# Kernel optimization log

Measured on AMD Instinct MI355X. Metric: run time of the kernel, lower is better.

The kernel has to match this reference:

```python
import jax, jax.numpy as jnp
import numpy as np

A, B, S, ADIM = 8, 8192, 128, 16   # n_agents, batch, state_dim, act_dim
H, HEADS = 512, 4                   # hidc, att_heads
D = H // HEADS                      # att_dim
EPS = 1e-5


def _ln(x):
    # LayerNorm over last dim, no affine (elementwise_affine=False), eps=1e-5
    m = jnp.mean(x, axis=-1, keepdims=True)
    v = jnp.var(x, axis=-1, keepdims=True)
    return (x - m) * jax.lax.rsqrt(v + EPS)


def setup_inputs() -> dict:
    key = jax.random.key(0)
    ks = jax.random.split(key, 16)
    sc = 0.02
    return {
        "states": jax.random.normal(ks[0], (A, B, S), jnp.float32),
        "actions": jax.random.normal(ks[1], (A, B, ADIM), jnp.float32),
        # per-agent state encoders (Encoder built with hidc in the source)
        "Ws_s": jax.random.normal(ks[2], (A, S, H), jnp.float32) * sc,
        "bs_s": jnp.zeros((A, H), jnp.float32),
        # per-agent state-action encoders
        "Ws_sa": jax.random.normal(ks[3], (A, S + ADIM, H), jnp.float32) * sc,
        "bs_sa": jnp.zeros((A, H), jnp.float32),
        # shared per-head key/value/selector projections
        "Wk": jax.random.normal(ks[4], (HEADS, H, D), jnp.float32) * sc,
        "Wv": jax.random.normal(ks[5], (HEADS, H, D), jnp.float32) * sc,
        "Wsel": jax.random.normal(ks[6], (HEADS, H, D), jnp.float32) * sc,
        "bsel": jnp.zeros((HEADS, D), jnp.float32),
        # per-agent critics: Linear(2H -> H), LeakyReLU, Linear(H -> ADIM)
        "Wc1": jax.random.normal(ks[7], (A, 2 * H, H), jnp.float32) * sc,
        "bc1": jnp.zeros((A, H), jnp.float32),
        "Wc2": jax.random.normal(ks[8], (A, H, ADIM), jnp.float32) * sc,
        "bc2": jnp.zeros((A, ADIM), jnp.float32),
    }


def reference(states, actions, Ws_s, bs_s, Ws_sa, bs_sa,
              Wk, Wv, Wsel, bsel, Wc1, bc1, Wc2, bc2):
    lrelu = jax.nn.leaky_relu  # slope 0.01 matches torch default

    # per-agent state encodings: [A,B,H]
    s_enc = lrelu(jnp.einsum('abs,ash->abh', _ln(states), Ws_s) + bs_s[:, None, :])

    # per-agent state-action encodings: [A,B,H]
    sa = jnp.concatenate([states, actions], axis=-1)
    sa_enc = lrelu(jnp.einsum('abs,ash->abh', _ln(sa), Ws_sa) + bs_sa[:, None, :])

    # per-head keys / values / selectors: [HEADS, A, B, D]
    keys = jnp.einsum('abh,khd->kabd', sa_enc, Wk)
    vals = jnp.einsum('abh,khd->kabd', sa_enc, Wv)
    sel = lrelu(jnp.einsum('abh,khd->kabd', sa_enc, Wsel) + bsel[:, None, None, :])

    # attention logits of agent i over agents j != i: [HEADS, A, A, B]
    logits = jnp.einsum('kibd,kjbd->kijb', sel, keys) / np.sqrt(D).astype(np.float32)
    self_mask = jnp.eye(A, dtype=bool)[None, :, :, None]
    w = jax.nn.softmax(jnp.where(self_mask, -jnp.inf, logits), axis=2)

    # attended values: [HEADS, A, B, D] -> concat heads -> [A, B, H]
    qvals = jnp.einsum('kijb,kjbd->kibd', w, vals)
    values = qvals.transpose(1, 2, 0, 3).reshape(A, B, H)

    # per-agent critics on concat(state_enc, attended values)
    cin = jnp.concatenate([s_enc, values], axis=-1)           # [A,B,2H]
    h1 = lrelu(jnp.einsum('abf,afh->abh', _ln(cin), Wc1) + bc1[:, None, :])
    all_qs = jnp.einsum('abh,aho->abo', h1, Wc2) + bc2[:, None, :]  # [A,B,ADIM]

    # Q of taken (argmax) action per agent: [A,B,1]
    idx = jnp.argmax(actions, axis=-1)
    q = jnp.take_along_axis(all_qs, idx[..., None], axis=-1)
    return q
```

## Files before the change

kernel.cpp:

```cpp
#include <hip/hip_runtime.h>
#include <hip/hip_bf16.h>
#include <math.h>


#define AN 8
#define BNB 8192
#define SN 128
#define ADN 16
#define HN 512
#define NHEADS 4
#define DN 128

typedef __hip_bfloat16 bf16;
typedef unsigned short u16;
typedef __attribute__((ext_vector_type(8))) short bf16x8;
typedef __attribute__((ext_vector_type(4))) float f32x4;

__device__ __forceinline__ float lrelu(float x){ return x > 0.f ? x : 0.01f*x; }
__device__ __forceinline__ float bflo(unsigned u){ return __uint_as_float(u << 16); }
__device__ __forceinline__ float bfhi(unsigned u){ return __uint_as_float(u & 0xffff0000u); }
__device__ __forceinline__ float bf2f(u16 u){ return __uint_as_float((unsigned)u << 16); }
__device__ __forceinline__ u16 f2bf(float v){
  union { bf16 h; u16 s; } cv; cv.h = __float2bfloat16(v); return cv.s;
}
__device__ __forceinline__ ushort4 f4bf(float4 v){
  ushort4 u; u.x=f2bf(v.x); u.y=f2bf(v.y); u.z=f2bf(v.z); u.w=f2bf(v.w); return u;
}

__device__ __forceinline__ void gload16(const u16* g, u16* l){
  __builtin_amdgcn_global_load_lds(
      (const __attribute__((address_space(1))) unsigned int*)(g),
      (__attribute__((address_space(3))) unsigned int*)(l), 16, 0, 0);
}

__global__ __launch_bounds__(256) void prep_kernel(
    const float* __restrict__ states, const float* __restrict__ actions,
    u16* __restrict__ sa_bf, float2* __restrict__ st_s, float2* __restrict__ st_sa,
    int* __restrict__ aip)
{
  const int lane = threadIdx.x & 63;
  const int r = blockIdx.x*4 + (threadIdx.x >> 6);
  float2 sv = ((const float2*)(states + (size_t)r*SN))[lane];
  float s1 = sv.x + sv.y, q1 = sv.x*sv.x + sv.y*sv.y;
  float2 av = make_float2(0.f, 0.f);
  if (lane < 8) av = ((const float2*)(actions + (size_t)r*ADN))[lane];
  float s2 = s1 + av.x + av.y, q2 = q1 + av.x*av.x + av.y*av.y;
  #pragma unroll
  for (int off=32; off; off>>=1){
    s1 += __shfl_xor(s1,off); q1 += __shfl_xor(q1,off);
    s2 += __shfl_xor(s2,off); q2 += __shfl_xor(q2,off);
  }
  float bv; int bi;
  if (lane < 8){
    if (av.x >= av.y){ bv = av.x; bi = 2*lane; } else { bv = av.y; bi = 2*lane+1; }
  } else { bv = -INFINITY; bi = 999; }
  #pragma unroll
  for (int off=1; off<8; off<<=1){
    float ov = __shfl_xor(bv, off); int oi = __shfl_xor(bi, off);
    if (ov > bv || (ov == bv && oi < bi)){ bv = ov; bi = oi; }
  }
  u16* row = sa_bf + (size_t)r*192;
  ushort2 p; p.x = f2bf(sv.x); p.y = f2bf(sv.y);
  *(ushort2*)(row + 2*lane) = p;
  if (lane < 8){
    ushort2 pa; pa.x = f2bf(av.x); pa.y = f2bf(av.y);
    *(ushort2*)(row + 128 + 2*lane) = pa;
  } else if (lane < 32){
    ushort2 z; z.x = 0; z.y = 0;
    *(ushort2*)(row + 128 + 2*lane) = z;
  }
  if (lane==0){
    float m1 = s1*(1.f/128.f), v1 = fmaxf(q1*(1.f/128.f)-m1*m1, 0.f);
    st_s[r] = make_float2(m1, rsqrtf(v1+1e-5f));
    float m2 = s2*(1.f/144.f), v2 = fmaxf(q2*(1.f/144.f)-m2*m2, 0.f);
    st_sa[r] = make_float2(m2, rsqrtf(v2+1e-5f));
    aip[r] = bi;
  }
}

__global__ __launch_bounds__(256) void transw_all_kernel(
    const float* __restrict__ Ws_s, const float* __restrict__ Ws_sa, const float* __restrict__ Wc1,
    const float* __restrict__ Wk, const float* __restrict__ Wv, const float* __restrict__ Wsel,
    u16* __restrict__ Wt_s, u16* __restrict__ Wt_sa, u16* __restrict__ Wt_c1, u16* __restrict__ Wt_p)
{
  __shared__ float t[32][33];
  int id = blockIdx.x;
  const float* in; u16* outp; int K, Kp; size_t zs; int gx;
  const int N = (id < 5376) ? 512 : 128;
  if (id < 512){            in=Ws_s;  outp=Wt_s;            K=128;  Kp=128;  zs=(size_t)512*128;  gx=4;  }
  else if (id < 1280){ id-=512;  in=Ws_sa; outp=Wt_sa;      K=144;  Kp=192;  zs=(size_t)512*192;  gx=6;  }
  else if (id < 5376){ id-=1280; in=Wc1;   outp=Wt_c1;      K=1024; Kp=1024; zs=(size_t)512*1024; gx=32; }
  else if (id < 5632){ id-=5376; in=Wk;    outp=Wt_p;            K=512; Kp=512; zs=(size_t)3*128*512; gx=16; }
  else if (id < 5888){ id-=5632; in=Wv;    outp=Wt_p+128*512;    K=512; Kp=512; zs=(size_t)3*128*512; gx=16; }
  else {               id-=5888; in=Wsel;  outp=Wt_p+2*128*512;  K=512; Kp=512; zs=(size_t)3*128*512; gx=16; }
  const int bx = id % gx; id /= gx;
  const int gy = N >> 5;
  const int by = id % gy;
  const int z  = id / gy;
  const int tx = threadIdx.x, ty = threadIdx.y;
  const int k0 = bx*32, n0 = by*32;
  const float* ip = in + (size_t)z*K*N;
  #pragma unroll
  for (int i=0;i<4;i++){
    int k = k0 + ty*4 + i;
    t[ty*4+i][tx] = (k < K) ? ip[(size_t)k*N + n0 + tx] : 0.f;
  }
  __syncthreads();
  u16* op = outp + (size_t)z*zs;
  #pragma unroll
  for (int i=0;i<4;i++){
    int n = n0 + ty*4 + i;
    op[(size_t)n*Kp + k0 + tx] = f2bf(t[tx][ty*4+i]);
  }
}

__global__ __launch_bounds__(256) void colsum_bf_kernel(
    const u16* __restrict__ Wt_s, const u16* __restrict__ Wt_sa, const u16* __restrict__ Wt_c1,
    float* __restrict__ cs_s, float* __restrict__ cs_sa, float* __restrict__ cs_c1)
{
  const int lane = threadIdx.x & 63;
  const int row = blockIdx.x*4 + (threadIdx.x >> 6);
  const int which = row >> 12; const int idx = row & 4095;
  const u16* W; int K; float* outp;
  if (which==0){ W = Wt_s;  K = 128;  outp = cs_s;  }
  else if (which==1){ W = Wt_sa; K = 192;  outp = cs_sa; }
  else { W = Wt_c1; K = 1024; outp = cs_c1; }
  const u16* p = W + (size_t)idx*K;
  float s = 0.f;
  for (int c = lane*8; c < K; c += 512){
    uint4 v = *(const uint4*)(p + c);
    const unsigned w4[4] = {v.x, v.y, v.z, v.w};
    #pragma unroll
    for (int t=0;t<4;t++) s += bflo(w4[t]) + bfhi(w4[t]);
  }
  #pragma unroll
  for (int off=32; off; off>>=1) s += __shfl_xor(s,off);
  if (lane==0) outp[idx] = s;
}

template<int MODE>
__global__ __launch_bounds__(256) void mfma_enc_kernel(
    const u16* __restrict__ Aa, const u16* __restrict__ Ab,
    const u16* __restrict__ Wt, const float* __restrict__ bias,
    const float2* __restrict__ stats, const float* __restrict__ csum,
    u16* __restrict__ outp,
    const float* __restrict__ Wc2, const float* __restrict__ bc2,
    const int* __restrict__ aip, float* __restrict__ qout)
{
  constexpr int K   = (MODE==0) ? 128 : (MODE==1 ? 192 : 1024);
  constexpr int LDA = (MODE==2) ? 512 : 192;
  constexpr int KP  = K;
  constexpr int SMEMN = (MODE==2) ? 20736 : 17408;
  __shared__ __align__(16) u16 smem[SMEMN];
  u16* As = smem;
  u16* Bs = smem + 8192;
  const int tid = threadIdx.x;
  const int w = tid>>6, lane = tid&63;
  const int wr = w>>1, wc = w&1;
  const int srow = lane>>3, skq = (lane&7)^srow;

  const int nwg = gridDim.x * gridDim.y;
  int id = blockIdx.y * gridDim.x + blockIdx.x;
  int swz = (id & 7) * (nwg >> 3) + (id >> 3);
  const int bx = swz % gridDim.x, by = swz / gridDim.x;

  const int m0 = by*128, n0c = bx*128;
  const int a = by >> 6;
  const u16* Wbase = Wt + (size_t)a*HN*KP;
  const int slotbase = (lane>>4) ^ (lane&7);
  f32x4 acc[4][4] = {};

  float* wc2l = nullptr; int* ail = nullptr;
  if constexpr (MODE==2){
    wc2l = (float*)(smem + 16384);
    ail  = (int*)(smem + 16384 + 4096);
    for (int e = tid; e < 2048; e += 256){
      const int aidx = e >> 7, col = e & 127;
      wc2l[e] = Wc2[((size_t)a*HN + n0c + col)*ADN + aidx];
    }
    if (tid < 128) ail[tid] = aip[m0 + tid];
  }

  for (int k0 = 0; k0 < K; k0 += 64){
    __syncthreads();
    const u16* asrc; int acol;
    if (MODE==2){ asrc = (k0 < 512) ? Aa : Ab; acol = k0 & 511; }
    else        { asrc = Aa; acol = k0; }
    #pragma unroll
    for (int t=0;t<4;t++){
      const int rr = w*32 + t*8;
      gload16(asrc  + (size_t)(m0  + rr + srow)*LDA + acol + skq*8, As + rr*64);
      gload16(Wbase + (size_t)(n0c + rr + srow)*KP  + k0   + skq*8, Bs + rr*64);
    }
    __syncthreads();
    #pragma unroll
    for (int ks=0; ks<2; ++ks){
      bf16x8 af[4], bv[4];
      const int so = ((slotbase ^ (ks<<2)))*8;
      #pragma unroll
      for (int mi=0;mi<4;mi++) af[mi] = *(const bf16x8*)&As[(wr*64+mi*16+(lane&15))*64 + so];
      #pragma unroll
      for (int ni=0;ni<4;ni++) bv[ni] = *(const bf16x8*)&Bs[(wc*64+ni*16+(lane&15))*64 + so];
      #pragma unroll
      for (int mi=0;mi<4;mi++)
        #pragma unroll
        for (int ni=0;ni<4;ni++)
          acc[mi][ni] = __builtin_amdgcn_mfma_f32_16x16x32_bf16(af[mi], bv[ni], acc[mi][ni], 0, 0, 0);
    }
  }

  __syncthreads();
  float csv[4], biv[4];
  #pragma unroll
  for (int ni=0;ni<4;ni++){
    const int col = n0c + wc*64 + ni*16 + (lane&15);
    csv[ni] = csum[a*HN + col];
    biv[ni] = bias[a*HN + col];
  }

  if constexpr (MODE==2){
    #pragma unroll
    for (int mi=0;mi<4;mi++){
      const int rbase = wr*64 + mi*16 + ((lane>>4)<<2);
      #pragma unroll
      for (int v=0; v<4; ++v){
        const int rl = rbase + v;
        const float2 st = stats[m0 + rl];
        const int aidx = ail[rl];
        float p = 0.f;
        #pragma unroll
        for (int ni=0;ni<4;ni++){
          const int coll = wc*64 + ni*16 + (lane&15);
          const float o = lrelu(st.y*(acc[mi][ni][v] - st.x*csv[ni]) + biv[ni]);
          p = fmaf(o, wc2l[aidx*128 + coll], p);
        }
        p += __shfl_xor(p,1); p += __shfl_xor(p,2);
        p += __shfl_xor(p,4); p += __shfl_xor(p,8);
        if ((lane&15)==0){
          if (n0c==0 && wc==0) p += bc2[a*ADN + aidx];
          atomicAdd(qout + m0 + rl, p);
        }
      }
    }
  } else {
    #pragma unroll
    for (int mi=0;mi<4;mi++){
      const int rl = wr*64 + mi*16 + ((lane>>4)<<2);
      #pragma unroll
      for (int v=0; v<4; ++v){
        const float2 st = stats[m0 + rl + v];
        #pragma unroll
        for (int ni=0;ni<4;ni++){
          const float o = lrelu(st.y*(acc[mi][ni][v] - st.x*csv[ni]) + biv[ni]);
          smem[(rl+v)*136 + wc*64 + ni*16 + (lane&15)] = f2bf(o);
        }
      }
    }
    __syncthreads();
    #pragma unroll
    for (int it=0; it<8; ++it){
      const int rl = it*16 + (tid>>4);
      const int ck = (tid&15)*8;
      const uint4 vv = *(const uint4*)&smem[rl*136 + ck];
      *(uint4*)(outp + (size_t)(m0+rl)*HN + n0c + ck) = vv;
    }
  }
}

__global__ __launch_bounds__(256) void mfma_proj_kernel(
    const u16* __restrict__ sa_enc, const u16* __restrict__ Wt_p,
    const float* __restrict__ bsel, u16* __restrict__ kvs, int head)
{
  __shared__ __align__(16) u16 smem[17408];
  u16* As = smem;
  u16* Bs = smem + 8192;
  const int tid = threadIdx.x;
  const int w = tid>>6, lane = tid&63;
  const int wr = w>>1, wc = w&1;
  const int srow = lane>>3, skq = (lane&7)^srow;

  const int nwg = gridDim.x * gridDim.y;
  int id = blockIdx.y * gridDim.x + blockIdx.x;
  int swz = (id & 7) * (nwg >> 3) + (id >> 3);
  const int t = swz % gridDim.x;
  const int m0 = (swz / gridDim.x) * 128;

  const u16* Wbase = Wt_p + (size_t)(head*3 + t)*DN*HN;
  const int slotbase = (lane>>4) ^ (lane&7);
  f32x4 acc[4][4] = {};

  for (int k0 = 0; k0 < HN; k0 += 64){
    __syncthreads();
    #pragma unroll
    for (int tt=0;tt<4;tt++){
      const int rr = w*32 + tt*8;
      gload16(sa_enc + (size_t)(m0 + rr + srow)*HN + k0 + skq*8, As + rr*64);
      gload16(Wbase  + (size_t)(rr + srow)*HN      + k0 + skq*8, Bs + rr*64);
    }
    __syncthreads();
    #pragma unroll
    for (int ks=0; ks<2; ++ks){
      bf16x8 af[4], bv[4];
      const int so = ((slotbase ^ (ks<<2)))*8;
      #pragma unroll
      for (int mi=0;mi<4;mi++) af[mi] = *(const bf16x8*)&As[(wr*64+mi*16+(lane&15))*64 + so];
      #pragma unroll
      for (int ni=0;ni<4;ni++) bv[ni] = *(const bf16x8*)&Bs[(wc*64+ni*16+(lane&15))*64 + so];
      #pragma unroll
      for (int mi=0;mi<4;mi++)
        #pragma unroll
        for (int ni=0;ni<4;ni++)
          acc[mi][ni] = __builtin_amdgcn_mfma_f32_16x16x32_bf16(af[mi], bv[ni], acc[mi][ni], 0, 0, 0);
    }
  }

  __syncthreads();
  const bool issel = (t == 2);
  float biv[4];
  #pragma unroll
  for (int ni=0;ni<4;ni++){
    const int col = wc*64 + ni*16 + (lane&15);
    biv[ni] = issel ? bsel[head*DN + col] : 0.f;
  }
  #pragma unroll
  for (int mi=0;mi<4;mi++){
    const int rl = wr*64 + mi*16 + ((lane>>4)<<2);
    #pragma unroll
    for (int v=0; v<4; ++v){
      #pragma unroll
      for (int ni=0;ni<4;ni++){
        float o = acc[mi][ni][v] + biv[ni];
        if (issel) o = lrelu(o);
        smem[(rl+v)*136 + wc*64 + ni*16 + (lane&15)] = f2bf(o);
      }
    }
  }
  __syncthreads();
  #pragma unroll
  for (int it=0; it<8; ++it){
    const int rl = it*16 + (tid>>4);
    const int ck = (tid&15)*8;
    const int r = m0 + rl;
    const int ar = r >> 13, b = r & (BNB-1);
    const uint4 vv = *(const uint4*)&smem[rl*136 + ck];
    *(uint4*)(kvs + (((size_t)t*BNB + b)*AN + ar)*DN + ck) = vv;
  }
}

__global__ __launch_bounds__(256) void attn_kernel(
    const u16* __restrict__ kvs, u16* __restrict__ values, int kh)
{
  __shared__ float lds[4][3232];
  const int lane = threadIdx.x & 63;
  const int wv   = threadIdx.x >> 6;
  float* selL = &lds[wv][0];
  float* keyL = &lds[wv][1056];
  float* valL = &lds[wv][2112];
  float* wL   = &lds[wv][3168];
  const int b = blockIdx.x*4 + wv;

  #pragma unroll
  for (int m=0;m<3;m++){
    const int t = (m==0) ? 2 : ((m==1) ? 0 : 1);
    float* dst = (m==0) ? selL : ((m==1) ? keyL : valL);
    const uint2* p = (const uint2*)(kvs + ((size_t)t*BNB + b)*(AN*DN));
    #pragma unroll
    for (int it=0; it<4; it++){
      uint2 u = p[it*64 + lane];
      int e = (it*64 + lane)*4;
      int j = e >> 7, d = e & 127;
      float4 f;
      f.x = bflo(u.x); f.y = bfhi(u.x); f.z = bflo(u.y); f.w = bfhi(u.y);
      *(float4*)&dst[j*132 + d] = f;
    }
  }
  __syncthreads();

  const int i = lane >> 3, j = lane & 7;
  float acc = 0.f;
  #pragma unroll 8
  for (int dq=0; dq<32; dq++){
    const float4 s4 = *(const float4*)&selL[i*132 + dq*4];
    const float4 k4 = *(const float4*)&keyL[j*132 + dq*4];
    acc += s4.x*k4.x + s4.y*k4.y + s4.z*k4.z + s4.w*k4.w;
  }
  float logit = acc * 0.08838834764831845f;
  if (i == j) logit = -INFINITY;
  float mx = logit;
  mx = fmaxf(mx, __shfl_xor(mx,1,8));
  mx = fmaxf(mx, __shfl_xor(mx,2,8));
  mx = fmaxf(mx, __shfl_xor(mx,4,8));
  const float e = __expf(logit - mx);
  float s = e;
  s += __shfl_xor(s,1,8);
  s += __shfl_xor(s,2,8);
  s += __shfl_xor(s,4,8);
  wL[i*8 + j] = e / s;
  __syncthreads();

  const int dq = lane & 7;
  float4 o[4];
  #pragma unroll
  for (int tt=0;tt<4;tt++) o[tt] = make_float4(0.f,0.f,0.f,0.f);
  #pragma unroll
  for (int jj=0;jj<8;jj++){
    const float wj = wL[i*8 + jj];
    #pragma unroll
    for (int tt=0;tt<4;tt++){
      const float4 v4 = *(const float4*)&valL[jj*132 + tt*32 + dq*4];
      o[tt].x += wj*v4.x; o[tt].y += wj*v4.y; o[tt].z += wj*v4.z; o[tt].w += wj*v4.w;
    }
  }
  u16* dst = values + ((size_t)i*BNB + b)*HN + kh*DN;
  #pragma unroll
  for (int tt=0;tt<4;tt++)
    *(ushort4*)(dst + tt*32 + dq*4) = f4bf(o[tt]);
}

__global__ __launch_bounds__(256) void stats_cin_kernel(
    const u16* __restrict__ s_enc, const u16* __restrict__ values, float2* __restrict__ st)
{
  const int lane = threadIdx.x & 63;
  const int r = blockIdx.x*4 + (threadIdx.x >> 6);
  const uint4* p1 = (const uint4*)(s_enc + (size_t)r*HN);
  const uint4* p2 = (const uint4*)(values + (size_t)r*HN);
  uint4 va = p1[lane];
  uint4 vb = p2[lane];
  float s=0.f, q=0.f;
  const unsigned wa[4] = {va.x, va.y, va.z, va.w};
  const unsigned wb[4] = {vb.x, vb.y, vb.z, vb.w};
  #pragma unroll
  for (int t=0;t<4;t++){
    float f0 = bflo(wa[t]), f1 = bfhi(wa[t]);
    float g0 = bflo(wb[t]), g1 = bfhi(wb[t]);
    s += f0+f1+g0+g1; q += f0*f0+f1*f1+g0*g0+g1*g1;
  }
  #pragma unroll
  for (int off=32; off; off>>=1){ s += __shfl_xor(s,off); q += __shfl_xor(q,off); }
  if (lane==0){
    float m = s*(1.f/1024.f); float v = fmaxf(q*(1.f/1024.f) - m*m, 0.f);
    st[r] = make_float2(m, rsqrtf(v + 1e-5f));
  }
}

extern "C" void kernel_launch(void* const* d_in, const int* in_sizes, int n_in,
                              void* d_out, int out_size, void* d_ws, size_t ws_size,
                              hipStream_t stream)
{
  (void)in_sizes; (void)n_in; (void)ws_size;
  const float* states  = (const float*)d_in[0];
  const float* actions = (const float*)d_in[1];
  const float* Ws_s    = (const float*)d_in[2];
  const float* bs_s    = (const float*)d_in[3];
  const float* Ws_sa   = (const float*)d_in[4];
  const float* bs_sa   = (const float*)d_in[5];
  const float* Wk      = (const float*)d_in[6];
  const float* Wv      = (const float*)d_in[7];
  const float* Wsel    = (const float*)d_in[8];
  const float* bsel    = (const float*)d_in[9];
  const float* Wc1     = (const float*)d_in[10];
  const float* bc1     = (const float*)d_in[11];
  const float* Wc2     = (const float*)d_in[12];
  const float* bc2     = (const float*)d_in[13];
  float* outp = (float*)d_out;

  char* ws = (char*)d_ws;
  size_t off = 0;
  auto alloc = [&](size_t n){ void* p = ws + off; off += (n + 255) & ~(size_t)255; return p; };
  u16*    slot1  = (u16*)   alloc((size_t)AN*BNB*HN*2);
  u16*    s_enc  = slot1;
  u16*    kvs    = slot1;
  u16*    sa_enc = (u16*)   alloc((size_t)AN*BNB*HN*2);
  u16*    values = (u16*)   alloc((size_t)AN*BNB*HN*2);
  u16*    sa_bf  = (u16*)   alloc((size_t)AN*BNB*192*2);
  u16*    Wt_s   = (u16*)   alloc((size_t)AN*HN*128*2);
  u16*    Wt_sa  = (u16*)   alloc((size_t)AN*HN*192*2);
  u16*    Wt_c1  = (u16*)   alloc((size_t)AN*HN*1024*2);
  u16*    Wt_p   = (u16*)   alloc((size_t)NHEADS*3*DN*HN*2);
  float2* st_s   = (float2*)alloc((size_t)AN*BNB*8);
  float2* st_sa  = (float2*)alloc((size_t)AN*BNB*8);
  float2* st_cin = (float2*)alloc((size_t)AN*BNB*8);
  float*  cs_s   = (float*) alloc((size_t)AN*HN*4);
  float*  cs_sa  = (float*) alloc((size_t)AN*HN*4);
  float*  cs_c1  = (float*) alloc((size_t)AN*HN*4);
  int*    aip    = (int*)   alloc((size_t)AN*BNB*4);

  hipMemsetAsync(d_out, 0, (size_t)out_size*4, stream);
  prep_kernel<<<dim3(AN*BNB/4), 256, 0, stream>>>(states, actions, sa_bf, st_s, st_sa, aip);
  transw_all_kernel<<<dim3(6144), dim3(32,8), 0, stream>>>(
      Ws_s, Ws_sa, Wc1, Wk, Wv, Wsel, Wt_s, Wt_sa, Wt_c1, Wt_p);
  colsum_bf_kernel<<<dim3(3*AN*HN/4), 256, 0, stream>>>(Wt_s, Wt_sa, Wt_c1, cs_s, cs_sa, cs_c1);

  mfma_enc_kernel<1><<<dim3(4,512), 256, 0, stream>>>(sa_bf, nullptr, Wt_sa, bs_sa, st_sa, cs_sa,
                                                      sa_enc, nullptr, nullptr, nullptr, nullptr);
  for (int kh = 0; kh < NHEADS; ++kh){
    mfma_proj_kernel<<<dim3(3,512), 256, 0, stream>>>(sa_enc, Wt_p, bsel, kvs, kh);
    attn_kernel<<<dim3(BNB/4), 256, 0, stream>>>(kvs, values, kh);
  }
  mfma_enc_kernel<0><<<dim3(4,512), 256, 0, stream>>>(sa_bf, nullptr, Wt_s, bs_s, st_s, cs_s,
                                                      s_enc, nullptr, nullptr, nullptr, nullptr);
  stats_cin_kernel<<<dim3(AN*BNB/4), 256, 0, stream>>>(s_enc, values, st_cin);
  mfma_enc_kernel<2><<<dim3(4,512), 256, 0, stream>>>(s_enc, values, Wt_c1, bc1, st_cin, cs_c1,
                                                      nullptr, Wc2, bc2, aip, outp);
}
```

Baseline: 471.7 us.

## Split critic GEMM into dedicated kernel and keep attention tiles in bf16 LDS

```diff
diff --git a/kernel.cpp b/kernel.cpp
--- a/kernel.cpp
+++ b/kernel.cpp
@@ -23,8 +23,8 @@
 __device__ __forceinline__ u16 f2bf(float v){
   union { bf16 h; u16 s; } cv; cv.h = __float2bfloat16(v); return cv.s;
 }
-__device__ __forceinline__ ushort4 f4bf(float4 v){
-  ushort4 u; u.x=f2bf(v.x); u.y=f2bf(v.y); u.z=f2bf(v.z); u.w=f2bf(v.w); return u;
+__device__ __forceinline__ unsigned pk2(float a, float b){
+  return (unsigned)f2bf(a) | ((unsigned)f2bf(b) << 16);
 }
 
 __device__ __forceinline__ void gload16(const u16* g, u16* l){
@@ -140,137 +140,14 @@
 
 template<int MODE>
 __global__ __launch_bounds__(256) void mfma_enc_kernel(
-    const u16* __restrict__ Aa, const u16* __restrict__ Ab,
+    const u16* __restrict__ Aa,
     const u16* __restrict__ Wt, const float* __restrict__ bias,
     const float2* __restrict__ stats, const float* __restrict__ csum,
-    u16* __restrict__ outp,
-    const float* __restrict__ Wc2, const float* __restrict__ bc2,
-    const int* __restrict__ aip, float* __restrict__ qout)
-{
-  constexpr int K   = (MODE==0) ? 128 : (MODE==1 ? 192 : 1024);
-  constexpr int LDA = (MODE==2) ? 512 : 192;
+    u16* __restrict__ outp)
+{
+  constexpr int K   = (MODE==0) ? 128 : 192;
+  constexpr int LDA = 192;
   constexpr int KP  = K;
-  constexpr int SMEMN = (MODE==2) ? 20736 : 17408;
-  __shared__ __align__(16) u16 smem[SMEMN];
-  u16* As = smem;
-  u16* Bs = smem + 8192;
-  const int tid = threadIdx.x;
-  const int w = tid>>6, lane = tid&63;
-  const int wr = w>>1, wc = w&1;
-  const int srow = lane>>3, skq = (lane&7)^srow;
-
-  const int nwg = gridDim.x * gridDim.y;
-  int id = blockIdx.y * gridDim.x + blockIdx.x;
-  int swz = (id & 7) * (nwg >> 3) + (id >> 3);
-  const int bx = swz % gridDim.x, by = swz / gridDim.x;
-
-  const int m0 = by*128, n0c = bx*128;
-  const int a = by >> 6;
-  const u16* Wbase = Wt + (size_t)a*HN*KP;
-  const int slotbase = (lane>>4) ^ (lane&7);
-  f32x4 acc[4][4] = {};
-
-  float* wc2l = nullptr; int* ail = nullptr;
-  if constexpr (MODE==2){
-    wc2l = (float*)(smem + 16384);
-    ail  = (int*)(smem + 16384 + 4096);
-    for (int e = tid; e < 2048; e += 256){
-      const int aidx = e >> 7, col = e & 127;
-      wc2l[e] = Wc2[((size_t)a*HN + n0c + col)*ADN + aidx];
-    }
-    if (tid < 128) ail[tid] = aip[m0 + tid];
-  }
-
-  for (int k0 = 0; k0 < K; k0 += 64){
-    __syncthreads();
-    const u16* asrc; int acol;
-    if (MODE==2){ asrc = (k0 < 512) ? Aa : Ab; acol = k0 & 511; }
-    else        { asrc = Aa; acol = k0; }
-    #pragma unroll
-    for (int t=0;t<4;t++){
-      const int rr = w*32 + t*8;
-      gload16(asrc  + (size_t)(m0  + rr + srow)*LDA + acol + skq*8, As + rr*64);
-      gload16(Wbase + (size_t)(n0c + rr + srow)*KP  + k0   + skq*8, Bs + rr*64);
-    }
-    __syncthreads();
-    #pragma unroll
-    for (int ks=0; ks<2; ++ks){
-      bf16x8 af[4], bv[4];
-      const int so = ((slotbase ^ (ks<<2)))*8;
-      #pragma unroll
-      for (int mi=0;mi<4;mi++) af[mi] = *(const bf16x8*)&As[(wr*64+mi*16+(lane&15))*64 + so];
-      #pragma unroll
-      for (int ni=0;ni<4;ni++) bv[ni] = *(const bf16x8*)&Bs[(wc*64+ni*16+(lane&15))*64 + so];
-      #pragma unroll
-      for (int mi=0;mi<4;mi++)
-        #pragma unroll
-        for (int ni=0;ni<4;ni++)
-          acc[mi][ni] = __builtin_amdgcn_mfma_f32_16x16x32_bf16(af[mi], bv[ni], acc[mi][ni], 0, 0, 0);
-    }
-  }
-
-  __syncthreads();
-  float csv[4], biv[4];
-  #pragma unroll
-  for (int ni=0;ni<4;ni++){
-    const int col = n0c + wc*64 + ni*16 + (lane&15);
-    csv[ni] = csum[a*HN + col];
-    biv[ni] = bias[a*HN + col];
-  }
-
-  if constexpr (MODE==2){
-    #pragma unroll
-    for (int mi=0;mi<4;mi++){
-      const int rbase = wr*64 + mi*16 + ((lane>>4)<<2);
-      #pragma unroll
-      for (int v=0; v<4; ++v){
-        const int rl = rbase + v;
-        const float2 st = stats[m0 + rl];
-        const int aidx = ail[rl];
-        float p = 0.f;
-        #pragma unroll
-        for (int ni=0;ni<4;ni++){
-          const int coll = wc*64 + ni*16 + (lane&15);
-          const float o = lrelu(st.y*(acc[mi][ni][v] - st.x*csv[ni]) + biv[ni]);
-          p = fmaf(o, wc2l[aidx*128 + coll], p);
-        }
-        p += __shfl_xor(p,1); p += __shfl_xor(p,2);
-        p += __shfl_xor(p,4); p += __shfl_xor(p,8);
-        if ((lane&15)==0){
-          if (n0c==0 && wc==0) p += bc2[a*ADN + aidx];
-          atomicAdd(qout + m0 + rl, p);
-        }
-      }
-    }
-  } else {
-    #pragma unroll
-    for (int mi=0;mi<4;mi++){
-      const int rl = wr*64 + mi*16 + ((lane>>4)<<2);
-      #pragma unroll
-      for (int v=0; v<4; ++v){
-        const float2 st = stats[m0 + rl + v];
-        #pragma unroll
-        for (int ni=0;ni<4;ni++){
-          const float o = lrelu(st.y*(acc[mi][ni][v] - st.x*csv[ni]) + biv[ni]);
-          smem[(rl+v)*136 + wc*64 + ni*16 + (lane&15)] = f2bf(o);
-        }
-      }
-    }
-    __syncthreads();
-    #pragma unroll
-    for (int it=0; it<8; ++it){
-      const int rl = it*16 + (tid>>4);
-      const int ck = (tid&15)*8;
-      const uint4 vv = *(const uint4*)&smem[rl*136 + ck];
-      *(uint4*)(outp + (size_t)(m0+rl)*HN + n0c + ck) = vv;
-    }
-  }
-}
-
-__global__ __launch_bounds__(256) void mfma_proj_kernel(
-    const u16* __restrict__ sa_enc, const u16* __restrict__ Wt_p,
-    const float* __restrict__ bsel, u16* __restrict__ kvs, int head)
-{
   __shared__ __align__(16) u16 smem[17408];
   u16* As = smem;
   u16* Bs = smem + 8192;
@@ -282,6 +159,178 @@
   const int nwg = gridDim.x * gridDim.y;
   int id = blockIdx.y * gridDim.x + blockIdx.x;
   int swz = (id & 7) * (nwg >> 3) + (id >> 3);
+  const int bx = swz % gridDim.x, by = swz / gridDim.x;
+
+  const int m0 = by*128, n0c = bx*128;
+  const int a = by >> 6;
+  const u16* Wbase = Wt + (size_t)a*HN*KP;
+  const int slotbase = (lane>>4) ^ (lane&7);
+  f32x4 acc[4][4] = {};
+
+  for (int k0 = 0; k0 < K; k0 += 64){
+    __syncthreads();
+    #pragma unroll
+    for (int t=0;t<4;t++){
+      const int rr = w*32 + t*8;
+      gload16(Aa    + (size_t)(m0  + rr + srow)*LDA + k0 + skq*8, As + rr*64);
+      gload16(Wbase + (size_t)(n0c + rr + srow)*KP  + k0 + skq*8, Bs + rr*64);
+    }
+    __syncthreads();
+    #pragma unroll
+    for (int ks=0; ks<2; ++ks){
+      bf16x8 af[4], bv[4];
+      const int so = ((slotbase ^ (ks<<2)))*8;
+      #pragma unroll
+      for (int mi=0;mi<4;mi++) af[mi] = *(const bf16x8*)&As[(wr*64+mi*16+(lane&15))*64 + so];
+      #pragma unroll
+      for (int ni=0;ni<4;ni++) bv[ni] = *(const bf16x8*)&Bs[(wc*64+ni*16+(lane&15))*64 + so];
+      #pragma unroll
+      for (int mi=0;mi<4;mi++)
+        #pragma unroll
+        for (int ni=0;ni<4;ni++)
+          acc[mi][ni] = __builtin_amdgcn_mfma_f32_16x16x32_bf16(af[mi], bv[ni], acc[mi][ni], 0, 0, 0);
+    }
+  }
+
+  __syncthreads();
+  float csv[4], biv[4];
+  #pragma unroll
+  for (int ni=0;ni<4;ni++){
+    const int col = n0c + wc*64 + ni*16 + (lane&15);
+    csv[ni] = csum[a*HN + col];
+    biv[ni] = bias[a*HN + col];
+  }
+  #pragma unroll
+  for (int mi=0;mi<4;mi++){
+    const int rl = wr*64 + mi*16 + ((lane>>4)<<2);
+    #pragma unroll
+    for (int v=0; v<4; ++v){
+      const float2 st = stats[m0 + rl + v];
+      #pragma unroll
+      for (int ni=0;ni<4;ni++){
+        const float o = lrelu(st.y*(acc[mi][ni][v] - st.x*csv[ni]) + biv[ni]);
+        smem[(rl+v)*136 + wc*64 + ni*16 + (lane&15)] = f2bf(o);
+      }
+    }
+  }
+  __syncthreads();
+  #pragma unroll
+  for (int it=0; it<8; ++it){
+    const int rl = it*16 + (tid>>4);
+    const int ck = (tid&15)*8;
+    const uint4 vv = *(const uint4*)&smem[rl*136 + ck];
+    *(uint4*)(outp + (size_t)(m0+rl)*HN + n0c + ck) = vv;
+  }
+}
+
+__global__ __launch_bounds__(256, 4) void mfma_critic_kernel(
+    const u16* __restrict__ Aa, const u16* __restrict__ Ab,
+    const u16* __restrict__ Wt, const float* __restrict__ bias,
+    const float2* __restrict__ stats, const float* __restrict__ csum,
+    const float* __restrict__ Wc2, const float* __restrict__ bc2,
+    const int* __restrict__ aip, float* __restrict__ qout)
+{
+  __shared__ __align__(16) u16 smem[18688];
+  u16* As = smem;
+  u16* Bs = smem + 8192;
+  u16* wc2l = smem + 16384;
+  int* ail  = (int*)(smem + 18432);
+  const int tid = threadIdx.x;
+  const int w = tid>>6, lane = tid&63;
+  const int wr = w>>1, wc = w&1;
+  const int srow = lane>>3, skq = (lane&7)^srow;
+
+  const int nwg = gridDim.x * gridDim.y;
+  int id = blockIdx.y * gridDim.x + blockIdx.x;
+  int swz = (id & 7) * (nwg >> 3) + (id >> 3);
+  const int bx = swz % gridDim.x, by = swz / gridDim.x;
+
+  const int m0 = by*128, n0c = bx*128;
+  const int a = by >> 6;
+  const u16* Wbase = Wt + (size_t)a*HN*1024;
+  const int slotbase = (lane>>4) ^ (lane&7);
+  f32x4 acc[4][4] = {};
+
+  const float* wsrc = Wc2 + ((size_t)a*HN + n0c)*ADN;
+  #pragma unroll
+  for (int i = 0; i < 8; ++i) wc2l[i*256 + tid] = f2bf(wsrc[i*256 + tid]);
+  if (tid < 128) ail[tid] = aip[m0 + tid];
+
+  for (int k0 = 0; k0 < 1024; k0 += 64){
+    __syncthreads();
+    const u16* asrc = (k0 < 512) ? Aa : Ab;
+    const int acol = k0 & 511;
+    #pragma unroll
+    for (int t=0;t<4;t++){
+      const int rr = w*32 + t*8;
+      gload16(asrc  + (size_t)(m0  + rr + srow)*HN   + acol + skq*8, As + rr*64);
+      gload16(Wbase + (size_t)(n0c + rr + srow)*1024 + k0   + skq*8, Bs + rr*64);
+    }
+    __syncthreads();
+    #pragma unroll
+    for (int ks=0; ks<2; ++ks){
+      bf16x8 af[4], bv[4];
+      const int so = ((slotbase ^ (ks<<2)))*8;
+      #pragma unroll
+      for (int mi=0;mi<4;mi++) af[mi] = *(const bf16x8*)&As[(wr*64+mi*16+(lane&15))*64 + so];
+      #pragma unroll
+      for (int ni=0;ni<4;ni++) bv[ni] = *(const bf16x8*)&Bs[(wc*64+ni*16+(lane&15))*64 + so];
+      #pragma unroll
+      for (int mi=0;mi<4;mi++)
+        #pragma unroll
+        for (int ni=0;ni<4;ni++)
+          acc[mi][ni] = __builtin_amdgcn_mfma_f32_16x16x32_bf16(af[mi], bv[ni], acc[mi][ni], 0, 0, 0);
+    }
+  }
+
+  __syncthreads();
+  float csv[4], biv[4];
+  #pragma unroll
+  for (int ni=0;ni<4;ni++){
+    const int col = n0c + wc*64 + ni*16 + (lane&15);
+    csv[ni] = csum[a*HN + col];
+    biv[ni] = bias[a*HN + col];
+  }
+  #pragma unroll
+  for (int mi=0;mi<4;mi++){
+    const int rbase = wr*64 + mi*16 + ((lane>>4)<<2);
+    #pragma unroll
+    for (int v=0; v<4; ++v){
+      const int rl = rbase + v;
+      const float2 st = stats[m0 + rl];
+      const int aidx = ail[rl];
+      float p = 0.f;
+      #pragma unroll
+      for (int ni=0;ni<4;ni++){
+        const int coll = wc*64 + ni*16 + (lane&15);
+        const float o = lrelu(st.y*(acc[mi][ni][v] - st.x*csv[ni]) + biv[ni]);
+        p = fmaf(o, bf2f(wc2l[coll*16 + aidx]), p);
+      }
+      p += __shfl_xor(p,1); p += __shfl_xor(p,2);
+      p += __shfl_xor(p,4); p += __shfl_xor(p,8);
+      if ((lane&15)==0){
+        if (n0c==0 && wc==0) p += bc2[a*ADN + aidx];
+        atomicAdd(qout + m0 + rl, p);
+      }
+    }
+  }
+}
+
+__global__ __launch_bounds__(256) void mfma_proj_kernel(
+    const u16* __restrict__ sa_enc, const u16* __restrict__ Wt_p,
+    const float* __restrict__ bsel, u16* __restrict__ kvs, int head)
+{
+  __shared__ __align__(16) u16 smem[17408];
+  u16* As = smem;
+  u16* Bs = smem + 8192;
+  const int tid = threadIdx.x;
+  const int w = tid>>6, lane = tid&63;
+  const int wr = w>>1, wc = w&1;
+  const int srow = lane>>3, skq = (lane&7)^srow;
+
+  const int nwg = gridDim.x * gridDim.y;
+  int id = blockIdx.y * gridDim.x + blockIdx.x;
+  int swz = (id & 7) * (nwg >> 3) + (id >> 3);
   const int t = swz % gridDim.x;
   const int m0 = (swz / gridDim.x) * 128;
 
@@ -348,73 +397,80 @@
 }
 
 __global__ __launch_bounds__(256) void attn_kernel(
-    const u16* __restrict__ kvs, u16* __restrict__ values, int kh)
-{
-  __shared__ float lds[4][3232];
+    const u16* __restrict__ kvs, u16* __restrict__ values, int head)
+{
+  __shared__ u16 tiles[4][3][1024];
   const int lane = threadIdx.x & 63;
   const int wv   = threadIdx.x >> 6;
-  float* selL = &lds[wv][0];
-  float* keyL = &lds[wv][1056];
-  float* valL = &lds[wv][2112];
-  float* wL   = &lds[wv][3168];
   const int b = blockIdx.x*4 + wv;
 
   #pragma unroll
-  for (int m=0;m<3;m++){
-    const int t = (m==0) ? 2 : ((m==1) ? 0 : 1);
-    float* dst = (m==0) ? selL : ((m==1) ? keyL : valL);
+  for (int t=0;t<3;t++){
     const uint2* p = (const uint2*)(kvs + ((size_t)t*BNB + b)*(AN*DN));
+    u16* dst = tiles[wv][t];
     #pragma unroll
     for (int it=0; it<4; it++){
-      uint2 u = p[it*64 + lane];
-      int e = (it*64 + lane)*4;
-      int j = e >> 7, d = e & 127;
-      float4 f;
-      f.x = bflo(u.x); f.y = bfhi(u.x); f.z = bflo(u.y); f.w = bfhi(u.y);
-      *(float4*)&dst[j*132 + d] = f;
-    }
-  }
-  __syncthreads();
+      const uint2 u = p[it*64 + lane];
+      const int e = (it*64 + lane)*4;
+      const int j = e >> 7, d = e & 127;
+      const int dsw = ((((d >> 3) ^ j) & 15) << 3) | (d & 7);
+      *(uint2*)&dst[j*128 + dsw] = u;
+    }
+  }
 
   const int i = lane >> 3, j = lane & 7;
-  float acc = 0.f;
-  #pragma unroll 8
-  for (int dq=0; dq<32; dq++){
-    const float4 s4 = *(const float4*)&selL[i*132 + dq*4];
-    const float4 k4 = *(const float4*)&keyL[j*132 + dq*4];
-    acc += s4.x*k4.x + s4.y*k4.y + s4.z*k4.z + s4.w*k4.w;
-  }
-  float logit = acc * 0.08838834764831845f;
+  const u16* selr = tiles[wv][2] + i*128;
+  const u16* keyr = tiles[wv][0] + j*128;
+  float dot = 0.f;
+  #pragma unroll
+  for (int c=0;c<16;c++){
+    const uint4 sv = *(const uint4*)&selr[((c ^ i) & 15) << 3];
+    const uint4 kv = *(const uint4*)&keyr[((c ^ j) & 15) << 3];
+    dot += bflo(sv.x)*bflo(kv.x) + bfhi(sv.x)*bfhi(kv.x);
+    dot += bflo(sv.y)*bflo(kv.y) + bfhi(sv.y)*bfhi(kv.y);
+    dot += bflo(sv.z)*bflo(kv.z) + bfhi(sv.z)*bfhi(kv.z);
+    dot += bflo(sv.w)*bflo(kv.w) + bfhi(sv.w)*bfhi(kv.w);
+  }
+  float logit = dot * 0.08838834764831845f;
   if (i == j) logit = -INFINITY;
   float mx = logit;
   mx = fmaxf(mx, __shfl_xor(mx,1,8));
   mx = fmaxf(mx, __shfl_xor(mx,2,8));
   mx = fmaxf(mx, __shfl_xor(mx,4,8));
   const float e = __expf(logit - mx);
-  float s = e;
-  s += __shfl_xor(s,1,8);
-  s += __shfl_xor(s,2,8);
-  s += __shfl_xor(s,4,8);
-  wL[i*8 + j] = e / s;
-  __syncthreads();
-
-  const int dq = lane & 7;
-  float4 o[4];
-  #pragma unroll
-  for (int tt=0;tt<4;tt++) o[tt] = make_float4(0.f,0.f,0.f,0.f);
-  #pragma unroll
-  for (int jj=0;jj<8;jj++){
-    const float wj = wL[i*8 + jj];
-    #pragma unroll
-    for (int tt=0;tt<4;tt++){
-      const float4 v4 = *(const float4*)&valL[jj*132 + tt*32 + dq*4];
-      o[tt].x += wj*v4.x; o[tt].y += wj*v4.y; o[tt].z += wj*v4.z; o[tt].w += wj*v4.w;
-    }
-  }
-  u16* dst = values + ((size_t)i*BNB + b)*HN + kh*DN;
-  #pragma unroll
-  for (int tt=0;tt<4;tt++)
-    *(ushort4*)(dst + tt*32 + dq*4) = f4bf(o[tt]);
+  float ssum = e;
+  ssum += __shfl_xor(ssum,1,8);
+  ssum += __shfl_xor(ssum,2,8);
+  ssum += __shfl_xor(ssum,4,8);
+  const float wgt = e / ssum;
+
+  const int dc = lane & 7;
+  float o[16];
+  #pragma unroll
+  for (int q = 0; q < 16; ++q) o[q] = 0.f;
+  #pragma unroll
+  for (int jj = 0; jj < 8; ++jj){
+    const float wj = __shfl(wgt, i*8 + jj);
+    const u16* valr = tiles[wv][1] + jj*128;
+    const uint4 v0 = *(const uint4*)&valr[(((2*dc)   ^ jj) & 15) << 3];
+    const uint4 v1 = *(const uint4*)&valr[(((2*dc+1) ^ jj) & 15) << 3];
+    o[0]  += wj*bflo(v0.x); o[1]  += wj*bfhi(v0.x);
+    o[2]  += wj*bflo(v0.y); o[3]  += wj*bfhi(v0.y);
+    o[4]  += wj*bflo(v0.z); o[5]  += wj*bfhi(v0.z);
+    o[6]  += wj*bflo(v0.w); o[7]  += wj*bfhi(v0.w);
+    o[8]  += wj*bflo(v1.x); o[9]  += wj*bfhi(v1.x);
+    o[10] += wj*bflo(v1.y); o[11] += wj*bfhi(v1.y);
+    o[12] += wj*bflo(v1.z); o[13] += wj*bfhi(v1.z);
+    o[14] += wj*bflo(v1.w); o[15] += wj*bfhi(v1.w);
+  }
+  uint4 p0, p1;
+  p0.x = pk2(o[0],o[1]);   p0.y = pk2(o[2],o[3]);
+  p0.z = pk2(o[4],o[5]);   p0.w = pk2(o[6],o[7]);
+  p1.x = pk2(o[8],o[9]);   p1.y = pk2(o[10],o[11]);
+  p1.z = pk2(o[12],o[13]); p1.w = pk2(o[14],o[15]);
+  u16* dst = values + ((size_t)i*BNB + b)*HN + head*DN + dc*16;
+  *(uint4*)dst = p0;
+  *(uint4*)(dst + 8) = p1;
 }
 
 __global__ __launch_bounds__(256) void stats_cin_kernel(
@@ -491,15 +547,13 @@
       Ws_s, Ws_sa, Wc1, Wk, Wv, Wsel, Wt_s, Wt_sa, Wt_c1, Wt_p);
   colsum_bf_kernel<<<dim3(3*AN*HN/4), 256, 0, stream>>>(Wt_s, Wt_sa, Wt_c1, cs_s, cs_sa, cs_c1);
 
-  mfma_enc_kernel<1><<<dim3(4,512), 256, 0, stream>>>(sa_bf, nullptr, Wt_sa, bs_sa, st_sa, cs_sa,
-                                                      sa_enc, nullptr, nullptr, nullptr, nullptr);
+  mfma_enc_kernel<1><<<dim3(4,512), 256, 0, stream>>>(sa_bf, Wt_sa, bs_sa, st_sa, cs_sa, sa_enc);
   for (int kh = 0; kh < NHEADS; ++kh){
     mfma_proj_kernel<<<dim3(3,512), 256, 0, stream>>>(sa_enc, Wt_p, bsel, kvs, kh);
     attn_kernel<<<dim3(BNB/4), 256, 0, stream>>>(kvs, values, kh);
   }
-  mfma_enc_kernel<0><<<dim3(4,512), 256, 0, stream>>>(sa_bf, nullptr, Wt_s, bs_s, st_s, cs_s,
-                                                      s_enc, nullptr, nullptr, nullptr, nullptr);
+  mfma_enc_kernel<0><<<dim3(4,512), 256, 0, stream>>>(sa_bf, Wt_s, bs_s, st_s, cs_s, s_enc);
   stats_cin_kernel<<<dim3(AN*BNB/4), 256, 0, stream>>>(s_enc, values, st_cin);
-  mfma_enc_kernel<2><<<dim3(4,512), 256, 0, stream>>>(s_enc, values, Wt_c1, bc1, st_cin, cs_c1,
-                                                      nullptr, Wc2, bc2, aip, outp);
-}
+  mfma_critic_kernel<<<dim3(4,512), 256, 0, stream>>>(s_enc, values, Wt_c1, bc1, st_cin, cs_c1,
+                                                      Wc2, bc2, aip, outp);
+}
```

Result: no change. 470.0 us (-0.4%).
